# Performance work log

Hardware: AMD Instinct MI355X
Metric: run time of the kernel (lower is better)

The kernel has to match this reference:

```python
import jax, jax.numpy as jnp
import numpy as np

B, C, O, H, W, K = 8, 64, 64, 96, 96, 3
PAD = 1


def setup_inputs() -> dict:
    key = jax.random.key(0)
    ks = jax.random.split(key, 5)
    x = jax.random.normal(ks[0], (B, C, H, W), jnp.float32)
    # small offset weights so sampled offsets stay O(1) pixel, like a trained net
    offset_w = jax.random.normal(ks[1], (2 * K * K, C, K, K), jnp.float32) * 0.01
    offset_b = jnp.zeros((2 * K * K,), jnp.float32)
    conv_w = jax.random.normal(ks[2], (O, C, K, K), jnp.float32) * (1.0 / np.sqrt(C * K * K))
    conv_b = jax.random.normal(ks[3], (O,), jnp.float32) * 0.01
    return {"x": x, "offset_w": offset_w, "offset_b": offset_b,
            "conv_w": conv_w, "conv_b": conv_b}


def _conv2d(x, w, b, pad):
    out = jax.lax.conv_general_dilated(
        x, w, window_strides=(1, 1), padding=[(pad, pad), (pad, pad)],
        dimension_numbers=("NCHW", "OIHW", "NCHW"))
    return out + b[None, :, None, None]


def _gather(x_flat, yi, xi):
    # x_flat: [B, C, H*W]; yi, xi: [B, K2, H, W] int32 sample indices
    valid = (yi >= 0) & (yi < H) & (xi >= 0) & (xi < W)
    idx = jnp.clip(yi, 0, H - 1) * W + jnp.clip(xi, 0, W - 1)
    idx_f = idx.reshape(idx.shape[0], -1)  # [B, K2*H*W]
    vals = jax.vmap(lambda xf, i: xf[:, i])(x_flat, idx_f)  # [B, C, K2*H*W]
    vals = vals.reshape(x_flat.shape[0], x_flat.shape[1], *idx.shape[1:])
    return vals * valid[:, None].astype(vals.dtype)  # zero padding outside


def _deform_conv2d(x, offset, w, b, pad):
    # Faithful to torchvision.ops.deform_conv2d (v1, 1 offset group, stride 1)
    K2 = K * K
    off = offset.reshape(offset.shape[0], K2, 2, H, W)
    dy, dx = off[:, :, 0], off[:, :, 1]  # (dy, dx) per kernel tap, torchvision order
    ky = jnp.repeat(jnp.arange(K), K).astype(x.dtype)  # row index i of tap k=i*K+j
    kx = jnp.tile(jnp.arange(K), K).astype(x.dtype)    # col index j
    # fractional sample positions [B, K2, H, W]
    py = jnp.arange(H, dtype=x.dtype)[None, None, :, None] - pad + ky[None, :, None, None] + dy
    px = jnp.arange(W, dtype=x.dtype)[None, None, None, :] - pad + kx[None, :, None, None] + dx
    y0 = jnp.floor(py)
    x0 = jnp.floor(px)
    wy = (py - y0)[:, None]  # broadcast over channels
    wx = (px - x0)[:, None]
    y0i = y0.astype(jnp.int32)
    x0i = x0.astype(jnp.int32)
    x_flat = x.reshape(x.shape[0], x.shape[1], H * W)
    g00 = _gather(x_flat, y0i, x0i)
    g01 = _gather(x_flat, y0i, x0i + 1)
    g10 = _gather(x_flat, y0i + 1, x0i)
    g11 = _gather(x_flat, y0i + 1, x0i + 1)
    # bilinear interp -> sampled patches [B, C, K2, H, W]
    sampled = (g00 * (1 - wy) * (1 - wx) + g01 * (1 - wy) * wx
               + g10 * wy * (1 - wx) + g11 * wy * wx)
    out = jnp.einsum("bckhw,ock->bohw", sampled, w.reshape(w.shape[0], w.shape[1], K2))
    return out + b[None, :, None, None]


def reference(x, offset_w, offset_b, conv_w, conv_b):
    offset = _conv2d(x, offset_w, offset_b, PAD)  # [B, 18, H, W]
    return _deform_conv2d(x, offset, conv_w, conv_b, PAD)
```

## Files before the change

kernel.cpp:

```cpp
#include <hip/hip_runtime.h>

#define Bb 8
#define Cc 64
#define Oo 64
#define Hh 96
#define Ww 96
#define HW 9216
#define NOFF 18

typedef __bf16 bf16_t;
typedef __bf16 bf16x2 __attribute__((ext_vector_type(2)));
typedef __bf16 bf16x8 __attribute__((ext_vector_type(8)));
typedef float  f32x4  __attribute__((ext_vector_type(4)));

#define XT_SZ   (Bb*HW*Cc)
#define WTPD_SZ (18*4*64*8)
#define WTPO_SZ (18*2*64*8)

__global__ void xpose_prep(const float* __restrict__ x, const float* __restrict__ cw,
                           const float* __restrict__ ow, bf16_t* __restrict__ xt,
                           bf16_t* __restrict__ wtpd, bf16_t* __restrict__ wtpo) {
    __shared__ float tile[64][65];
    int bid = blockIdx.x;
    if (bid < 1152) {
        int b    = bid / 144;
        int t0   = (bid % 144) * 64;
        int lane = threadIdx.x & 63;
        int sub  = threadIdx.x >> 6;
        const float* xb = x + (size_t)b * Cc * HW;
        #pragma unroll
        for (int i = 0; i < 16; ++i) {
            int c = sub * 16 + i;
            tile[c][lane] = xb[c * HW + t0 + lane];
        }
        __syncthreads();
        bf16_t* xtb = xt + ((size_t)b * HW + t0) * Cc;
        int half = lane >> 5, cpair = lane & 31;
        #pragma unroll
        for (int i = 0; i < 8; ++i) {
            int hw = sub * 16 + half * 8 + i;
            bf16x2 v;
            v[0] = (bf16_t)tile[cpair * 2][hw];
            v[1] = (bf16_t)tile[cpair * 2 + 1][hw];
            *(bf16x2*)&xtb[hw * Cc + cpair * 2] = v;
        }
    } else if (bid < 1170) {
        int n = (bid - 1152) * 256 + threadIdx.x;
        int t = n >> 8; int rem = n & 255; int mt = rem >> 6; int l = rem & 63;
        int o = mt * 16 + (l & 15);
        int kbase = t * 32 + ((l >> 4) & 3) * 8;
        bf16x8 v;
        #pragma unroll
        for (int j = 0; j < 8; ++j) {
            int kidx = kbase + j; int k = kidx >> 6; int c = kidx & 63;
            v[j] = (bf16_t)cw[(o * 64 + c) * 9 + k];
        }
        *(bf16x8*)&wtpd[n * 8] = v;
    } else {
        int n = (bid - 1170) * 256 + threadIdx.x;
        int t = n >> 7; int rem = n & 127; int mt = rem >> 6; int l = rem & 63;
        int oc = mt * 16 + (l & 15);
        int kbase = t * 32 + ((l >> 4) & 3) * 8;
        bf16x8 v;
        #pragma unroll
        for (int j = 0; j < 8; ++j) {
            int kidx = kbase + j; int k = kidx >> 6; int c = kidx & 63;
            v[j] = (oc < NOFF) ? (bf16_t)ow[(oc * 64 + c) * 9 + k] : (bf16_t)0.f;
        }
        *(bf16x8*)&wtpo[n * 8] = v;
    }
}

__global__ __launch_bounds__(256, 3) void fused_dcn(const bf16_t* __restrict__ xt,
        const bf16_t* __restrict__ wtpo, const bf16_t* __restrict__ wtpd,
        const float* __restrict__ ob, const float* __restrict__ cb,
        float* __restrict__ out) {
    __shared__ float offbuf[64 * 20];
    __shared__ bf16_t Sa[4][16 * 72];

    int bid = blockIdx.x;
    int b = bid & 7;
    int t8 = bid >> 3;
    int h0 = (t8 / 12) * 8, w0 = (t8 % 12) * 8;
    int tid = threadIdx.x, lane = tid & 63, q = tid >> 6;
    int cg = lane & 7, prow = lane >> 3;
    int cb8 = cg * 8;
    bf16_t* myS = &Sa[q][0];
    int bbase = b * HW;

    int pl[2], ph[2], pw[2];
    #pragma unroll
    for (int i = 0; i < 2; ++i) {
        pl[i] = q * 16 + i * 8 + prow;
        ph[i] = h0 + q * 2 + i;
        pw[i] = w0 + prow;
    }

    const bf16x8* wtpo_v = (const bf16x8*)wtpo;
    const bf16x8* wtpd_v = (const bf16x8*)wtpd;

    {
        f32x4 acc1[2];
        #pragma unroll
        for (int mt = 0; mt < 2; ++mt)
            #pragma unroll
            for (int r = 0; r < 4; ++r) {
                int oc = mt * 16 + ((lane >> 4) & 3) * 4 + r;
                acc1[mt][r] = (oc < NOFF) ? ob[oc] : 0.f;
            }
        bf16x8 g[2][2];
        auto issue = [&](int k, bf16x8 (&gg)[2]) {
            const int ky = k / 3, kx = k % 3;
            #pragma unroll
            for (int i = 0; i < 2; ++i) {
                int y = ph[i] - 1 + ky, x = pw[i] - 1 + kx;
                bool valid = (y >= 0) && (y < Hh) && (x >= 0) && (x < Ww);
                bf16x8 v;
                #pragma unroll
                for (int j = 0; j < 8; ++j) v[j] = (bf16_t)0.f;
                if (valid) v = *(const bf16x8*)(xt + ((bbase + y * Ww + x) * Cc + cb8));
                gg[i] = v;
            }
        };
        issue(0, g[0]);
        issue(1, g[1]);
        #pragma unroll
        for (int k = 0; k < 9; ++k) {
            #pragma unroll
            for (int i = 0; i < 2; ++i)
                *(bf16x8*)&myS[(i * 8 + prow) * 72 + cb8] = g[k & 1][i];
            if (k < 7) issue(k + 2, g[k & 1]);
            #pragma unroll
            for (int s = 0; s < 2; ++s) {
                bf16x8 bfrag = *(bf16x8*)&myS[(lane & 15) * 72 + s * 32 + ((lane >> 4) & 3) * 8];
                int t = k * 2 + s;
                #pragma unroll
                for (int mt = 0; mt < 2; ++mt) {
                    bf16x8 afrag = wtpo_v[(t * 2 + mt) * 64 + lane];
                    acc1[mt] = __builtin_amdgcn_mfma_f32_16x16x32_bf16(afrag, bfrag, acc1[mt], 0, 0, 0);
                }
            }
        }
        #pragma unroll
        for (int mt = 0; mt < 2; ++mt)
            #pragma unroll
            for (int r = 0; r < 4; ++r) {
                int oc = mt * 16 + ((lane >> 4) & 3) * 4 + r;
                if (oc < NOFF)
                    offbuf[(q * 16 + (lane & 15)) * 20 + oc] = acc1[mt][r];
            }
    }
    __syncthreads();

    f32x4 acc[4];
    #pragma unroll
    for (int mt = 0; mt < 4; ++mt)
        #pragma unroll
        for (int r = 0; r < 4; ++r)
            acc[mt][r] = cb[mt * 16 + ((lane >> 4) & 3) * 4 + r];

    bf16x8 g[2][2][4];
    float w4[2][2][4];
    auto issue = [&](int k, bf16x8 (&gg)[2][4], float (&ww)[2][4]) {
        const int ky = k / 3, kx = k % 3;
        #pragma unroll
        for (int i = 0; i < 2; ++i) {
            float2 od = *(float2*)&offbuf[pl[i] * 20 + 2 * k];
            float py = (float)(ph[i] - 1 + ky) + od.x;
            float px = (float)(pw[i] - 1 + kx) + od.y;
            float fy = floorf(py), fx = floorf(px);
            float wy = py - fy, wx = px - fx;
            int y0 = (int)fy, x0 = (int)fx;
            int y1 = y0 + 1, x1 = x0 + 1;
            bool vy0 = (unsigned)y0 < (unsigned)Hh, vy1 = (unsigned)y1 < (unsigned)Hh;
            bool vx0 = (unsigned)x0 < (unsigned)Ww, vx1 = (unsigned)x1 < (unsigned)Ww;
            int y0c = min(max(y0, 0), Hh - 1), y1c = min(max(y1, 0), Hh - 1);
            int x0c = min(max(x0, 0), Ww - 1), x1c = min(max(x1, 0), Ww - 1);
            ww[i][0] = (vy0 && vx0) ? (1.f - wy) * (1.f - wx) : 0.f;
            ww[i][1] = (vy0 && vx1) ? (1.f - wy) * wx : 0.f;
            ww[i][2] = (vy1 && vx0) ? wy * (1.f - wx) : 0.f;
            ww[i][3] = (vy1 && vx1) ? wy * wx : 0.f;
            int r0 = (bbase + y0c * Ww) * Cc, r1 = (bbase + y1c * Ww) * Cc;
            gg[i][0] = *(const bf16x8*)(xt + r0 + x0c * Cc + cb8);
            gg[i][1] = *(const bf16x8*)(xt + r0 + x1c * Cc + cb8);
            gg[i][2] = *(const bf16x8*)(xt + r1 + x0c * Cc + cb8);
            gg[i][3] = *(const bf16x8*)(xt + r1 + x1c * Cc + cb8);
        }
    };
    issue(0, g[0], w4[0]);
    issue(1, g[1], w4[1]);
    #pragma unroll
    for (int k = 0; k < 9; ++k) {
        int par = k & 1;
        #pragma unroll
        for (int i = 0; i < 2; ++i) {
            bf16x8 v;
            #pragma unroll
            for (int j = 0; j < 8; ++j) {
                float s = (float)g[par][i][0][j] * w4[par][i][0]
                        + (float)g[par][i][1][j] * w4[par][i][1]
                        + (float)g[par][i][2][j] * w4[par][i][2]
                        + (float)g[par][i][3][j] * w4[par][i][3];
                v[j] = (bf16_t)s;
            }
            *(bf16x8*)&myS[(i * 8 + prow) * 72 + cb8] = v;
        }
        if (k < 7) issue(k + 2, g[par], w4[par]);
        #pragma unroll
        for (int s = 0; s < 2; ++s) {
            bf16x8 bfrag = *(bf16x8*)&myS[(lane & 15) * 72 + s * 32 + ((lane >> 4) & 3) * 8];
            int t = k * 2 + s;
            #pragma unroll
            for (int mt = 0; mt < 4; ++mt) {
                bf16x8 afrag = wtpd_v[(t * 4 + mt) * 64 + lane];
                acc[mt] = __builtin_amdgcn_mfma_f32_16x16x32_bf16(afrag, bfrag, acc[mt], 0, 0, 0);
            }
        }
    }
    #pragma unroll
    for (int mt = 0; mt < 4; ++mt)
        #pragma unroll
        for (int r = 0; r < 4; ++r) {
            int o = mt * 16 + ((lane >> 4) & 3) * 4 + r;
            int pix = q * 16 + (lane & 15);
            out[(b * Oo + o) * HW + (h0 + (pix >> 3)) * Ww + w0 + (pix & 7)] = acc[mt][r];
        }
}

extern "C" void kernel_launch(void* const* d_in, const int* in_sizes, int n_in,
                              void* d_out, int out_size, void* d_ws, size_t ws_size,
                              hipStream_t stream) {
    const float* x  = (const float*)d_in[0];
    const float* ow = (const float*)d_in[1];
    const float* ob = (const float*)d_in[2];
    const float* cw = (const float*)d_in[3];
    const float* cb = (const float*)d_in[4];
    float* out = (float*)d_out;

    bf16_t* xt   = (bf16_t*)d_ws;
    bf16_t* wtpd = xt + XT_SZ;
    bf16_t* wtpo = wtpd + WTPD_SZ;

    xpose_prep<<<1179, 256, 0, stream>>>(x, cw, ow, xt, wtpd, wtpo);
    fused_dcn <<<1152, 256, 0, stream>>>(xt, wtpo, wtpd, ob, cb, out);
}
```

Baseline: 114.5 us.

## Halve block to two waves, each handling two pixel groups sharing weight fragments

The block shrinks from four waves to two, and each wave now processes two 16-pixel groups. Each weight A-fragment loaded from global memory feeds two MFMAs, which halves weight-fragment traffic per pixel. To fit the extra accumulators and gathers in registers, gather prefetch depth drops from two taps ahead to one. Fewer waves per block and a shallower prefetch may expose more gather latency and reduce occupancy, since registers per thread grow.

New measurement: 115.2 us. No clear change (+0.6%).

```diff
diff --git a/kernel.cpp b/kernel.cpp
--- a/kernel.cpp
+++ b/kernel.cpp
@@ -71,12 +71,12 @@
     }
 }
 
-__global__ __launch_bounds__(256, 3) void fused_dcn(const bf16_t* __restrict__ xt,
+__global__ __launch_bounds__(128, 3) void fused_dcn(const bf16_t* __restrict__ xt,
         const bf16_t* __restrict__ wtpo, const bf16_t* __restrict__ wtpd,
         const float* __restrict__ ob, const float* __restrict__ cb,
         float* __restrict__ out) {
     __shared__ float offbuf[64 * 20];
-    __shared__ bf16_t Sa[4][16 * 72];
+    __shared__ bf16_t Sa[2][2][16 * 72];
 
     int bid = blockIdx.x;
     int b = bid & 7;
@@ -85,146 +85,173 @@
     int tid = threadIdx.x, lane = tid & 63, q = tid >> 6;
     int cg = lane & 7, prow = lane >> 3;
     int cb8 = cg * 8;
-    bf16_t* myS = &Sa[q][0];
+    int quad = (lane >> 4) & 3;
+    int p16 = lane & 15;
     int bbase = b * HW;
 
-    int pl[2], ph[2], pw[2];
-    #pragma unroll
-    for (int i = 0; i < 2; ++i) {
-        pl[i] = q * 16 + i * 8 + prow;
-        ph[i] = h0 + q * 2 + i;
-        pw[i] = w0 + prow;
-    }
+    int pl[2][2], ph[2][2], pw[2][2];
+    #pragma unroll
+    for (int u = 0; u < 2; ++u)
+        #pragma unroll
+        for (int i = 0; i < 2; ++i) {
+            int grp = q * 2 + u;
+            pl[u][i] = grp * 16 + i * 8 + prow;
+            ph[u][i] = h0 + grp * 2 + i;
+            pw[u][i] = w0 + prow;
+        }
 
     const bf16x8* wtpo_v = (const bf16x8*)wtpo;
     const bf16x8* wtpd_v = (const bf16x8*)wtpd;
 
     {
-        f32x4 acc1[2];
-        #pragma unroll
-        for (int mt = 0; mt < 2; ++mt)
-            #pragma unroll
-            for (int r = 0; r < 4; ++r) {
-                int oc = mt * 16 + ((lane >> 4) & 3) * 4 + r;
-                acc1[mt][r] = (oc < NOFF) ? ob[oc] : 0.f;
-            }
-        bf16x8 g[2][2];
-        auto issue = [&](int k, bf16x8 (&gg)[2]) {
+        f32x4 acc1[2][2];
+        #pragma unroll
+        for (int u = 0; u < 2; ++u)
+            #pragma unroll
+            for (int mt = 0; mt < 2; ++mt)
+                #pragma unroll
+                for (int r = 0; r < 4; ++r) {
+                    int oc = mt * 16 + quad * 4 + r;
+                    acc1[u][mt][r] = (oc < NOFF) ? ob[oc] : 0.f;
+                }
+        bf16x8 g1[2][2];
+        auto issue1 = [&](int k) {
             const int ky = k / 3, kx = k % 3;
             #pragma unroll
-            for (int i = 0; i < 2; ++i) {
-                int y = ph[i] - 1 + ky, x = pw[i] - 1 + kx;
-                bool valid = (y >= 0) && (y < Hh) && (x >= 0) && (x < Ww);
-                bf16x8 v;
-                #pragma unroll
-                for (int j = 0; j < 8; ++j) v[j] = (bf16_t)0.f;
-                if (valid) v = *(const bf16x8*)(xt + ((bbase + y * Ww + x) * Cc + cb8));
-                gg[i] = v;
-            }
+            for (int u = 0; u < 2; ++u)
+                #pragma unroll
+                for (int i = 0; i < 2; ++i) {
+                    int y = ph[u][i] - 1 + ky, x = pw[u][i] - 1 + kx;
+                    bool valid = (y >= 0) && (y < Hh) && (x >= 0) && (x < Ww);
+                    bf16x8 v;
+                    #pragma unroll
+                    for (int j = 0; j < 8; ++j) v[j] = (bf16_t)0.f;
+                    if (valid) v = *(const bf16x8*)(xt + ((bbase + y * Ww + x) * Cc + cb8));
+                    g1[u][i] = v;
+                }
         };
-        issue(0, g[0]);
-        issue(1, g[1]);
+        issue1(0);
         #pragma unroll
         for (int k = 0; k < 9; ++k) {
             #pragma unroll
-            for (int i = 0; i < 2; ++i)
-                *(bf16x8*)&myS[(i * 8 + prow) * 72 + cb8] = g[k & 1][i];
-            if (k < 7) issue(k + 2, g[k & 1]);
+            for (int u = 0; u < 2; ++u)
+                #pragma unroll
+                for (int i = 0; i < 2; ++i)
+                    *(bf16x8*)&Sa[q][u][(i * 8 + prow) * 72 + cb8] = g1[u][i];
+            if (k < 8) issue1(k + 1);
             #pragma unroll
             for (int s = 0; s < 2; ++s) {
-                bf16x8 bfrag = *(bf16x8*)&myS[(lane & 15) * 72 + s * 32 + ((lane >> 4) & 3) * 8];
+                bf16x8 bfrag[2];
+                #pragma unroll
+                for (int u = 0; u < 2; ++u)
+                    bfrag[u] = *(bf16x8*)&Sa[q][u][p16 * 72 + s * 32 + quad * 8];
                 int t = k * 2 + s;
                 #pragma unroll
                 for (int mt = 0; mt < 2; ++mt) {
                     bf16x8 afrag = wtpo_v[(t * 2 + mt) * 64 + lane];
-                    acc1[mt] = __builtin_amdgcn_mfma_f32_16x16x32_bf16(afrag, bfrag, acc1[mt], 0, 0, 0);
-                }
-            }
-        }
-        #pragma unroll
-        for (int mt = 0; mt < 2; ++mt)
-            #pragma unroll
-            for (int r = 0; r < 4; ++r) {
-                int oc = mt * 16 + ((lane >> 4) & 3) * 4 + r;
-                if (oc < NOFF)
-                    offbuf[(q * 16 + (lane & 15)) * 20 + oc] = acc1[mt][r];
-            }
+                    #pragma unroll
+                    for (int u = 0; u < 2; ++u)
+                        acc1[u][mt] = __builtin_amdgcn_mfma_f32_16x16x32_bf16(afrag, bfrag[u], acc1[u][mt], 0, 0, 0);
+                }
+            }
+        }
+        #pragma unroll
+        for (int u = 0; u < 2; ++u)
+            #pragma unroll
+            for (int mt = 0; mt < 2; ++mt)
+                #pragma unroll
+                for (int r = 0; r < 4; ++r) {
+                    int oc = mt * 16 + quad * 4 + r;
+                    if (oc < NOFF)
+                        offbuf[((q * 2 + u) * 16 + p16) * 20 + oc] = acc1[u][mt][r];
+                }
     }
     __syncthreads();
 
-    f32x4 acc[4];
-    #pragma unroll
-    for (int mt = 0; mt < 4; ++mt)
-        #pragma unroll
-        for (int r = 0; r < 4; ++r)
-            acc[mt][r] = cb[mt * 16 + ((lane >> 4) & 3) * 4 + r];
+    f32x4 acc[2][4];
+    #pragma unroll
+    for (int u = 0; u < 2; ++u)
+        #pragma unroll
+        for (int mt = 0; mt < 4; ++mt)
+            #pragma unroll
+            for (int r = 0; r < 4; ++r)
+                acc[u][mt][r] = cb[mt * 16 + quad * 4 + r];
 
     bf16x8 g[2][2][4];
     float w4[2][2][4];
-    auto issue = [&](int k, bf16x8 (&gg)[2][4], float (&ww)[2][4]) {
+    auto issue = [&](int k) {
         const int ky = k / 3, kx = k % 3;
         #pragma unroll
-        for (int i = 0; i < 2; ++i) {
-            float2 od = *(float2*)&offbuf[pl[i] * 20 + 2 * k];
-            float py = (float)(ph[i] - 1 + ky) + od.x;
-            float px = (float)(pw[i] - 1 + kx) + od.y;
-            float fy = floorf(py), fx = floorf(px);
-            float wy = py - fy, wx = px - fx;
-            int y0 = (int)fy, x0 = (int)fx;
-            int y1 = y0 + 1, x1 = x0 + 1;
-            bool vy0 = (unsigned)y0 < (unsigned)Hh, vy1 = (unsigned)y1 < (unsigned)Hh;
-            bool vx0 = (unsigned)x0 < (unsigned)Ww, vx1 = (unsigned)x1 < (unsigned)Ww;
-            int y0c = min(max(y0, 0), Hh - 1), y1c = min(max(y1, 0), Hh - 1);
-            int x0c = min(max(x0, 0), Ww - 1), x1c = min(max(x1, 0), Ww - 1);
-            ww[i][0] = (vy0 && vx0) ? (1.f - wy) * (1.f - wx) : 0.f;
-            ww[i][1] = (vy0 && vx1) ? (1.f - wy) * wx : 0.f;
-            ww[i][2] = (vy1 && vx0) ? wy * (1.f - wx) : 0.f;
-            ww[i][3] = (vy1 && vx1) ? wy * wx : 0.f;
-            int r0 = (bbase + y0c * Ww) * Cc, r1 = (bbase + y1c * Ww) * Cc;
-            gg[i][0] = *(const bf16x8*)(xt + r0 + x0c * Cc + cb8);
-            gg[i][1] = *(const bf16x8*)(xt + r0 + x1c * Cc + cb8);
-            gg[i][2] = *(const bf16x8*)(xt + r1 + x0c * Cc + cb8);
-            gg[i][3] = *(const bf16x8*)(xt + r1 + x1c * Cc + cb8);
-        }
+        for (int u = 0; u < 2; ++u)
+            #pragma unroll
+            for (int i = 0; i < 2; ++i) {
+                float2 od = *(float2*)&offbuf[pl[u][i] * 20 + 2 * k];
+                float py = (float)(ph[u][i] - 1 + ky) + od.x;
+                float px = (float)(pw[u][i] - 1 + kx) + od.y;
+                float fy = floorf(py), fx = floorf(px);
+                float wy = py - fy, wx = px - fx;
+                int y0 = (int)fy, x0 = (int)fx;
+                int y1 = y0 + 1, x1 = x0 + 1;
+                bool vy0 = (unsigned)y0 < (unsigned)Hh, vy1 = (unsigned)y1 < (unsigned)Hh;
+                bool vx0 = (unsigned)x0 < (unsigned)Ww, vx1 = (unsigned)x1 < (unsigned)Ww;
+                int y0c = min(max(y0, 0), Hh - 1), y1c = min(max(y1, 0), Hh - 1);
+                int x0c = min(max(x0, 0), Ww - 1), x1c = min(max(x1, 0), Ww - 1);
+                w4[u][i][0] = (vy0 && vx0) ? (1.f - wy) * (1.f - wx) : 0.f;
+                w4[u][i][1] = (vy0 && vx1) ? (1.f - wy) * wx : 0.f;
+                w4[u][i][2] = (vy1 && vx0) ? wy * (1.f - wx) : 0.f;
+                w4[u][i][3] = (vy1 && vx1) ? wy * wx : 0.f;
+                int r0 = (bbase + y0c * Ww) * Cc, r1 = (bbase + y1c * Ww) * Cc;
+                g[u][i][0] = *(const bf16x8*)(xt + r0 + x0c * Cc + cb8);
+                g[u][i][1] = *(const bf16x8*)(xt + r0 + x1c * Cc + cb8);
+                g[u][i][2] = *(const bf16x8*)(xt + r1 + x0c * Cc + cb8);
+                g[u][i][3] = *(const bf16x8*)(xt + r1 + x1c * Cc + cb8);
+            }
     };
-    issue(0, g[0], w4[0]);
-    issue(1, g[1], w4[1]);
+    issue(0);
     #pragma unroll
     for (int k = 0; k < 9; ++k) {
-        int par = k & 1;
-        #pragma unroll
-        for (int i = 0; i < 2; ++i) {
-            bf16x8 v;
-            #pragma unroll
-            for (int j = 0; j < 8; ++j) {
-                float s = (float)g[par][i][0][j] * w4[par][i][0]
-                        + (float)g[par][i][1][j] * w4[par][i][1]
-                        + (float)g[par][i][2][j] * w4[par][i][2]
-                        + (float)g[par][i][3][j] * w4[par][i][3];
-                v[j] = (bf16_t)s;
-            }
-            *(bf16x8*)&myS[(i * 8 + prow) * 72 + cb8] = v;
-        }
-        if (k < 7) issue(k + 2, g[par], w4[par]);
+        #pragma unroll
+        for (int u = 0; u < 2; ++u)
+            #pragma unroll
+            for (int i = 0; i < 2; ++i) {
+                bf16x8 v;
+                #pragma unroll
+                for (int j = 0; j < 8; ++j) {
+                    float s = (float)g[u][i][0][j] * w4[u][i][0]
+                            + (float)g[u][i][1][j] * w4[u][i][1]
+                            + (float)g[u][i][2][j] * w4[u][i][2]
+                            + (float)g[u][i][3][j] * w4[u][i][3];
+                    v[j] = (bf16_t)s;
+                }
+                *(bf16x8*)&Sa[q][u][(i * 8 + prow) * 72 + cb8] = v;
+            }
+        if (k < 8) issue(k + 1);
         #pragma unroll
         for (int s = 0; s < 2; ++s) {
-            bf16x8 bfrag = *(bf16x8*)&myS[(lane & 15) * 72 + s * 32 + ((lane >> 4) & 3) * 8];
+            bf16x8 bfrag[2];
+            #pragma unroll
+            for (int u = 0; u < 2; ++u)
+                bfrag[u] = *(bf16x8*)&Sa[q][u][p16 * 72 + s * 32 + quad * 8];
             int t = k * 2 + s;
             #pragma unroll
             for (int mt = 0; mt < 4; ++mt) {
                 bf16x8 afrag = wtpd_v[(t * 4 + mt) * 64 + lane];
-                acc[mt] = __builtin_amdgcn_mfma_f32_16x16x32_bf16(afrag, bfrag, acc[mt], 0, 0, 0);
+                #pragma unroll
+                for (int u = 0; u < 2; ++u)
+                    acc[u][mt] = __builtin_amdgcn_mfma_f32_16x16x32_bf16(afrag, bfrag[u], acc[u][mt], 0, 0, 0);
             }
         }
     }
     #pragma unroll
-    for (int mt = 0; mt < 4; ++mt)
-        #pragma unroll
-        for (int r = 0; r < 4; ++r) {
-            int o = mt * 16 + ((lane >> 4) & 3) * 4 + r;
-            int pix = q * 16 + (lane & 15);
-            out[(b * Oo + o) * HW + (h0 + (pix >> 3)) * Ww + w0 + (pix & 7)] = acc[mt][r];
-        }
+    for (int u = 0; u < 2; ++u)
+        #pragma unroll
+        for (int mt = 0; mt < 4; ++mt)
+            #pragma unroll
+            for (int r = 0; r < 4; ++r) {
+                int o = mt * 16 + quad * 4 + r;
+                int pix = (q * 2 + u) * 16 + p16;
+                out[(b * Oo + o) * HW + (h0 + (pix >> 3)) * Ww + w0 + (pix & 7)] = acc[u][mt][r];
+            }
 }
 
 extern "C" void kernel_launch(void* const* d_in, const int* in_sizes, int n_in,
@@ -242,5 +269,5 @@
     bf16_t* wtpo = wtpd + WTPD_SZ;
 
     xpose_prep<<<1179, 256, 0, stream>>>(x, cw, ow, xt, wtpd, wtpo);
-    fused_dcn <<<1152, 256, 0, stream>>>(xt, wtpo, wtpd, ob, cb, out);
+    fused_dcn <<<1152, 128, 0, stream>>>(xt, wtpo, wtpd, ob, cb, out);
 }
```
